# Kernel tuning notes

Hardware: AMD Instinct MI355X
Metric: run time of the kernel (lower is better)

The kernel has to match this reference:

```python
import jax, jax.numpy as jnp
import numpy as np

BN_EPS = 1e-5


def setup_inputs() -> dict:
    key = jax.random.key(0)
    ks = jax.random.split(key, 6)
    b, c_out, c_high = 8, 256, 512
    h1 = w1 = 64
    h2 = w2 = 32
    return {
        "fms_low": jax.random.normal(ks[0], (b, c_out, h1, w1), jnp.float32),
        "fms_high": jax.random.normal(ks[1], (b, c_high, h2, w2), jnp.float32),
        "w_conv": jax.random.normal(ks[2], (c_out, c_high), jnp.float32) * (1.0 / np.sqrt(c_high)),
        "bn_gamma": jnp.ones((c_out,), jnp.float32),
        "bn_beta": jnp.zeros((c_out,), jnp.float32),
        "bn_mean": jnp.zeros((c_out,), jnp.float32),
        "bn_var": jnp.ones((c_out,), jnp.float32),
        "fc1_w": jax.random.normal(ks[3], (c_out // 4, c_out), jnp.float32) * (1.0 / np.sqrt(c_out)),
        "fc1_b": jnp.zeros((c_out // 4,), jnp.float32),
        "fc2_w": jax.random.normal(ks[4], (c_out // 4, c_out), jnp.float32) * (1.0 / np.sqrt(c_out)),
        "fc2_b": jnp.zeros((c_out // 4,), jnp.float32),
        "scale": jax.random.normal(ks[5], (1,), jnp.float32),
    }


def reference(fms_low, fms_high, w_conv, bn_gamma, bn_beta, bn_mean, bn_var,
              fc1_w, fc1_b, fc2_w, fc2_b, scale):
    b, c, h1, w1 = fms_low.shape
    # conv_high: 1x1 conv (no bias) + BN (inference) + ReLU
    x = jnp.einsum('bchw,oc->bohw', fms_high, w_conv)  # [b, 256, h2, w2]
    inv = bn_gamma / jnp.sqrt(bn_var + BN_EPS)
    x = x * inv[None, :, None, None] + (bn_beta - bn_mean * inv)[None, :, None, None]
    x = jax.nn.relu(x)
    # raw row-major reshapes, matching torch .view(b, -1, C)
    feat_low = fms_low.reshape(b, -1, c)    # [b, N_low, 256]
    feat_high = x.reshape(b, -1, c)         # [b, N_high, 256]
    mid_low = feat_low @ fc1_w.T + fc1_b    # [b, N_low, 64]
    mid_high = feat_high @ fc2_w.T + fc2_b  # [b, N_high, 64]
    energy = jnp.einsum('bnd,bmd->bnm', mid_low, mid_high)  # [b, N_low, N_high]
    attn = jax.nn.softmax(energy, axis=-1)
    # bmm(feat_high^T, attn^T) -> [b, 256, N_low]
    mid = jnp.einsum('bmc,bnm->bcn', feat_high, attn).reshape(b, c, h1, w1)
    return scale[0] * mid
```

## Files before the change

kernel.cpp:

```cpp
#include <hip/hip_runtime.h>
#include <hip/hip_bf16.h>

typedef __bf16 v8bf __attribute__((ext_vector_type(8)));
typedef float  v4f  __attribute__((ext_vector_type(4)));

typedef __attribute__((address_space(3))) void       lds_vd;
typedef __attribute__((address_space(1))) const void gbl_vd;

#define MFMA16(a, b, c) __builtin_amdgcn_mfma_f32_16x16x32_bf16(a, b, c, 0, 0, 0)

__device__ __forceinline__ void split_hl(float v, __bf16* h, __bf16* l) {
    __bf16 hh = (__bf16)v;
    *h = hh;
    *l = (__bf16)(v - (float)hh);
}

__device__ __forceinline__ int swz_idx(int row, int col) {
    return row * 64 + ((((col >> 3) ^ (row & 7))) << 3) + (col & 7);
}
__device__ __forceinline__ const __bf16* frag_ptr(const __bf16* base, int row, int g) {
    return base + row * 64 + ((g ^ (row & 7)) << 3);
}


__global__ __launch_bounds__(256) void k_conv(
    const float* __restrict__ FH, const float* __restrict__ W,
    const float* __restrict__ gamma, const float* __restrict__ beta,
    const float* __restrict__ mean, const float* __restrict__ var,
    __bf16* __restrict__ Xhi, __bf16* __restrict__ Xlo, __bf16* __restrict__ VT)
{
    __shared__ __align__(16) __bf16 Ah[64 * 64];
    __shared__ __align__(16) __bf16 Al[64 * 64];
    __shared__ __align__(16) __bf16 Bh[64 * 64];
    __shared__ __align__(16) __bf16 Bl[64 * 64];
    __shared__ float invl[64], shl[64];

    const int tid = threadIdx.x, lane = tid & 63, w = tid >> 6;
    const int l15 = lane & 15, quad = lane >> 4;
    const int u0 = blockIdx.x * 16, o0 = blockIdx.y * 64, b = blockIdx.z;
    const float* FHb = FH + (size_t)b * 524288;

    if (tid < 64) {
        const int o = o0 + tid;
        const float iv = gamma[o] * rsqrtf(var[o] + 1e-5f);
        invl[tid] = iv;
        shl[tid] = beta[o] - mean[o] * iv;
    }

    const int ao = tid >> 2, aseg = tid & 3;
    float wreg[16], freg[16];
    {
        const float* wp = W + (size_t)(o0 + ao) * 512 + aseg * 16;
        #pragma unroll
        for (int q = 0; q < 4; ++q) {
            float4 f = ((const float4*)wp)[q];
            wreg[4*q] = f.x; wreg[4*q+1] = f.y; wreg[4*q+2] = f.z; wreg[4*q+3] = f.w;
        }
        const float* fp = FHb + (size_t)lane * 1024 + w * 256 + u0;
        #pragma unroll
        for (int q = 0; q < 4; ++q) {
            float4 f = ((const float4*)fp)[q];
            freg[4*q] = f.x; freg[4*q+1] = f.y; freg[4*q+2] = f.z; freg[4*q+3] = f.w;
        }
    }

    v4f acc[2][2];
    #pragma unroll
    for (int i = 0; i < 2; ++i)
        #pragma unroll
        for (int j = 0; j < 2; ++j) { v4f z = {0.f,0.f,0.f,0.f}; acc[i][j] = z; }
    const int oh = w >> 1, nh = w & 1;

    for (int ch = 0; ch < 8; ++ch) {
        if (ch) __syncthreads();
        #pragma unroll
        for (int z = 0; z < 2; ++z) {
            v8bf hv, lv;
            #pragma unroll
            for (int e = 0; e < 8; ++e) {
                __bf16 h, l; split_hl(wreg[8*z + e], &h, &l);
                hv[e] = h; lv[e] = l;
            }
            const int gi = (2*aseg + z) ^ (ao & 7);
            *(v8bf*)(Ah + ao*64 + (gi << 3)) = hv;
            *(v8bf*)(Al + ao*64 + (gi << 3)) = lv;
        }
        #pragma unroll
        for (int ul = 0; ul < 16; ++ul) {
            __bf16 h, l; split_hl(freg[ul], &h, &l);
            const int idx = (w*16 + ul)*64 + (((lane >> 3) ^ (ul & 7)) << 3) + (lane & 7);
            Bh[idx] = h; Bl[idx] = l;
        }
        __syncthreads();
        if (ch < 7) {
            const int c1 = (ch + 1) * 64;
            const float* wp = W + (size_t)(o0 + ao) * 512 + c1 + aseg * 16;
            #pragma unroll
            for (int q = 0; q < 4; ++q) {
                float4 f = ((const float4*)wp)[q];
                wreg[4*q] = f.x; wreg[4*q+1] = f.y; wreg[4*q+2] = f.z; wreg[4*q+3] = f.w;
            }
            const float* fp = FHb + (size_t)(c1 + lane) * 1024 + w * 256 + u0;
            #pragma unroll
            for (int q = 0; q < 4; ++q) {
                float4 f = ((const float4*)fp)[q];
                freg[4*q] = f.x; freg[4*q+1] = f.y; freg[4*q+2] = f.z; freg[4*q+3] = f.w;
            }
        }
        #pragma unroll
        for (int ks = 0; ks < 2; ++ks) {
            const int g = 4*ks + quad;
            v8bf a_h[2], a_l[2], b_h[2], b_l[2];
            #pragma unroll
            for (int i = 0; i < 2; ++i) {
                const int row = oh*32 + i*16 + l15;
                a_h[i] = *(const v8bf*)frag_ptr(Ah, row, g);
                a_l[i] = *(const v8bf*)frag_ptr(Al, row, g);
            }
            #pragma unroll
            for (int j = 0; j < 2; ++j) {
                const int row = nh*32 + j*16 + l15;
                b_h[j] = *(const v8bf*)frag_ptr(Bh, row, g);
                b_l[j] = *(const v8bf*)frag_ptr(Bl, row, g);
            }
            #pragma unroll
            for (int i = 0; i < 2; ++i)
                #pragma unroll
                for (int j = 0; j < 2; ++j) {
                    acc[i][j] = MFMA16(a_h[i], b_h[j], acc[i][j]);
                    acc[i][j] = MFMA16(a_h[i], b_l[j], acc[i][j]);
                    acc[i][j] = MFMA16(a_l[i], b_h[j], acc[i][j]);
                }
        }
    }
    __syncthreads();

    #pragma unroll
    for (int i = 0; i < 2; ++i)
        #pragma unroll
        for (int j = 0; j < 2; ++j)
            #pragma unroll
            for (int r = 0; r < 4; ++r) {
                const int row = oh*32 + i*16 + quad*4 + r;
                const int col = nh*32 + j*16 + l15;
                float v = acc[i][j][r] * invl[row] + shl[row];
                v = fmaxf(v, 0.f);
                __bf16 h, l; split_hl(v, &h, &l);
                const int idx = swz_idx(row, col);
                Ah[idx] = h; Al[idx] = l;
            }
    __syncthreads();
    {
        const int o = tid >> 2, pv = tid & 3;
        const size_t gbase = ((size_t)b*256 + o0 + o) * 1024 + pv*256 + u0;
        #pragma unroll
        for (int z = 0; z < 2; ++z) {
            const int gi = (2*pv + z) ^ (o & 7);
            v8bf h = *(v8bf*)(Ah + o*64 + (gi << 3));
            v8bf l = *(v8bf*)(Al + o*64 + (gi << 3));
            *(v8bf*)(Xhi + gbase + z*8) = h;
            *(v8bf*)(Xlo + gbase + z*8) = l;
        }
    }
    {
        const int ul = tid >> 4, s = tid & 15;
        __bf16 tmp[16];
        #pragma unroll
        for (int k = 0; k < 16; ++k) {
            const int m = s*16 + k;
            const int row = m >> 2;
            const int col = (m & 3)*16 + ul;
            tmp[k] = Ah[swz_idx(row, col)];
        }
        __bf16* vp = VT + ((size_t)b*256 + u0 + ul) * 1024 + 4*o0 + s*16;
        *(v8bf*)(vp)     = *(v8bf*)(tmp);
        *(v8bf*)(vp + 8) = *(v8bf*)(tmp + 8);
    }
}

__global__ __launch_bounds__(256) void k_proj32(
    const float* __restrict__ Feat, const float* __restrict__ Wfc,
    const float* __restrict__ bfc,
    __bf16* __restrict__ Ohi, __bf16* __restrict__ Olo)
{
    __shared__ __align__(16) __bf16 Bh[64 * 256];
    __shared__ __align__(16) __bf16 Bl[64 * 256];
    __shared__ __align__(16) __bf16 Eo[4][16 * 64];

    const int tid = threadIdx.x, lane = tid & 63, w = tid >> 6;
    const int l15 = lane & 15, quad = lane >> 4;
    const int r0 = blockIdx.x * 64;
    const int row = r0 + w*16 + l15;

    const float* ap = Feat + (size_t)row * 256 + quad * 8;
    float acur[8], anxt[8];
    {
        float4 f0 = ((const float4*)ap)[0];
        float4 f1 = ((const float4*)ap)[1];
        acur[0]=f0.x; acur[1]=f0.y; acur[2]=f0.z; acur[3]=f0.w;
        acur[4]=f1.x; acur[5]=f1.y; acur[6]=f1.z; acur[7]=f1.w;
    }

    {
        const int n = tid >> 2, q4 = tid & 3, n7 = n & 7;
        const float* wp = Wfc + (size_t)n * 256 + q4 * 64;
        #pragma unroll
        for (int z = 0; z < 8; ++z) {
            float4 f0 = ((const float4*)wp)[2*z];
            float4 f1 = ((const float4*)wp)[2*z + 1];
            float w8[8] = {f0.x, f0.y, f0.z, f0.w, f1.x, f1.y, f1.z, f1.w};
            v8bf hv, lv;
            #pragma unroll
            for (int e = 0; e < 8; ++e) {
                __bf16 h, l; split_hl(w8[e], &h, &l);
                hv[e] = h; lv[e] = l;
            }
            const int gsw = (q4*8 + z) ^ n7;
            *(v8bf*)(Bh + n*256 + gsw*8) = hv;
            *(v8bf*)(Bl + n*256 + gsw*8) = lv;
        }
    }
    __syncthreads();

    v4f acc[4];
    #pragma unroll
    for (int j = 0; j < 4; ++j) { v4f z = {0.f,0.f,0.f,0.f}; acc[j] = z; }

    const int l7 = l15 & 7;
    const __bf16* bh_base = Bh + l15*256;
    const __bf16* bl_base = Bl + l15*256;

    #pragma unroll
    for (int kc = 0; kc < 8; ++kc) {
        if (kc < 7) {
            float4 f0 = ((const float4*)(ap + (kc+1)*32))[0];
            float4 f1 = ((const float4*)(ap + (kc+1)*32))[1];
            anxt[0]=f0.x; anxt[1]=f0.y; anxt[2]=f0.z; anxt[3]=f0.w;
            anxt[4]=f1.x; anxt[5]=f1.y; anxt[6]=f1.z; anxt[7]=f1.w;
        }
        v8bf ah, al;
        #pragma unroll
        for (int e = 0; e < 8; ++e) {
            __bf16 h, l; split_hl(acur[e], &h, &l);
            ah[e] = h; al[e] = l;
        }
        const int goff = (((kc*4 + quad) ^ l7) << 3);
        #pragma unroll
        for (int j = 0; j < 4; ++j) {
            v8bf bh = *(const v8bf*)(bh_base + j*4096 + goff);
            v8bf bl = *(const v8bf*)(bl_base + j*4096 + goff);
            acc[j] = MFMA16(ah, bh, acc[j]);
            acc[j] = MFMA16(ah, bl, acc[j]);
            acc[j] = MFMA16(al, bh, acc[j]);
        }
        #pragma unroll
        for (int e = 0; e < 8; ++e) acur[e] = anxt[e];
    }

    __bf16* eo = &Eo[w][0];
    __bf16 lb[4][4];
    #pragma unroll
    for (int j = 0; j < 4; ++j) {
        const float bias = bfc[j*16 + l15];
        #pragma unroll
        for (int r = 0; r < 4; ++r) {
            __bf16 h, l; split_hl(acc[j][r] + bias, &h, &l);
            lb[j][r] = l;
            eo[swz_idx(quad*4 + r, j*16 + l15)] = h;
        }
    }
    const size_t orow = (size_t)row * 64;
    #pragma unroll
    for (int z = 0; z < 2; ++z) {
        const int gi = (2*quad + z) ^ l7;
        *(v8bf*)(Ohi + orow + quad*16 + z*8) = *(v8bf*)(eo + l15*64 + gi*8);
    }
    #pragma unroll
    for (int j = 0; j < 4; ++j)
        #pragma unroll
        for (int r = 0; r < 4; ++r)
            eo[swz_idx(quad*4 + r, j*16 + l15)] = lb[j][r];
    #pragma unroll
    for (int z = 0; z < 2; ++z) {
        const int gi = (2*quad + z) ^ l7;
        *(v8bf*)(Olo + orow + quad*16 + z*8) = *(v8bf*)(eo + l15*64 + gi*8);
    }
}

__global__ __launch_bounds__(256) void k_projbf(
    const __bf16* __restrict__ Fhi, const __bf16* __restrict__ Flo,
    const float* __restrict__ Wfc, const float* __restrict__ bfc,
    __bf16* __restrict__ Ohi, __bf16* __restrict__ Olo)
{
    __shared__ __align__(16) __bf16 Bh[64 * 256];
    __shared__ __align__(16) __bf16 Bl[64 * 256];
    __shared__ __align__(16) __bf16 Eo[4][16 * 64];

    const int tid = threadIdx.x, lane = tid & 63, w = tid >> 6;
    const int l15 = lane & 15, quad = lane >> 4;
    const int r0 = blockIdx.x * 64;
    const int row = r0 + w*16 + l15;

    const __bf16* fh = Fhi + (size_t)row * 256 + quad * 8;
    const __bf16* fl = Flo + (size_t)row * 256 + quad * 8;
    v8bf ah = *(const v8bf*)(fh);
    v8bf al = *(const v8bf*)(fl);

    {
        const int n = tid >> 2, q4 = tid & 3, n7 = n & 7;
        const float* wp = Wfc + (size_t)n * 256 + q4 * 64;
        #pragma unroll
        for (int z = 0; z < 8; ++z) {
            float4 f0 = ((const float4*)wp)[2*z];
            float4 f1 = ((const float4*)wp)[2*z + 1];
            float w8[8] = {f0.x, f0.y, f0.z, f0.w, f1.x, f1.y, f1.z, f1.w};
            v8bf hv, lv;
            #pragma unroll
            for (int e = 0; e < 8; ++e) {
                __bf16 h, l; split_hl(w8[e], &h, &l);
                hv[e] = h; lv[e] = l;
            }
            const int gsw = (q4*8 + z) ^ n7;
            *(v8bf*)(Bh + n*256 + gsw*8) = hv;
            *(v8bf*)(Bl + n*256 + gsw*8) = lv;
        }
    }
    __syncthreads();

    v4f acc[4];
    #pragma unroll
    for (int j = 0; j < 4; ++j) { v4f z = {0.f,0.f,0.f,0.f}; acc[j] = z; }

    const int l7 = l15 & 7;
    const __bf16* bh_base = Bh + l15*256;
    const __bf16* bl_base = Bl + l15*256;

    #pragma unroll
    for (int kc = 0; kc < 8; ++kc) {
        v8bf anh, anl;
        if (kc < 7) {
            anh = *(const v8bf*)(fh + (kc+1)*32);
            anl = *(const v8bf*)(fl + (kc+1)*32);
        }
        const int goff = (((kc*4 + quad) ^ l7) << 3);
        #pragma unroll
        for (int j = 0; j < 4; ++j) {
            v8bf bh = *(const v8bf*)(bh_base + j*4096 + goff);
            v8bf bl = *(const v8bf*)(bl_base + j*4096 + goff);
            acc[j] = MFMA16(ah, bh, acc[j]);
            acc[j] = MFMA16(ah, bl, acc[j]);
            acc[j] = MFMA16(al, bh, acc[j]);
        }
        if (kc < 7) { ah = anh; al = anl; }
    }

    __bf16* eo = &Eo[w][0];
    __bf16 lb[4][4];
    #pragma unroll
    for (int j = 0; j < 4; ++j) {
        const float bias = bfc[j*16 + l15];
        #pragma unroll
        for (int r = 0; r < 4; ++r) {
            __bf16 h, l; split_hl(acc[j][r] + bias, &h, &l);
            lb[j][r] = l;
            eo[swz_idx(quad*4 + r, j*16 + l15)] = h;
        }
    }
    const size_t orow = (size_t)row * 64;
    #pragma unroll
    for (int z = 0; z < 2; ++z) {
        const int gi = (2*quad + z) ^ l7;
        *(v8bf*)(Ohi + orow + quad*16 + z*8) = *(v8bf*)(eo + l15*64 + gi*8);
    }
    #pragma unroll
    for (int j = 0; j < 4; ++j)
        #pragma unroll
        for (int r = 0; r < 4; ++r)
            eo[swz_idx(quad*4 + r, j*16 + l15)] = lb[j][r];
    #pragma unroll
    for (int z = 0; z < 2; ++z) {
        const int gi = (2*quad + z) ^ l7;
        *(v8bf*)(Olo + orow + quad*16 + z*8) = *(v8bf*)(eo + l15*64 + gi*8);
    }
}

__global__ __launch_bounds__(512, 4) void k_attn(
    const __bf16* __restrict__ MLhi, const __bf16* __restrict__ MLlo,
    const __bf16* __restrict__ MHhi, const __bf16* __restrict__ MHlo,
    const __bf16* __restrict__ VT,
    const float* __restrict__ scale_p,
    float* __restrict__ out)
{
    __shared__ __align__(16) __bf16 Khi[2][32 * 64];
    __shared__ __align__(16) __bf16 Klo[2][32 * 64];
    __shared__ __align__(16) __bf16 Vs [2][256 * 32];
    __shared__ __align__(16) __bf16 Ps [2][4][16 * 32];
    __shared__ float lsh[2][4][16];

    const int tid = threadIdx.x, lane = tid & 63, w = tid >> 6;
    const int l15 = lane & 15, quad = lane >> 4;
    const int b = blockIdx.x & 7, qtb = blockIdx.x >> 3;
    const int q0 = qtb * 64;
    const int qt = w & 3, mb = w >> 2;

    v8bf qhi[2], qlo[2];
    {
        const __bf16* qp  = MLhi + ((size_t)(b*4096 + q0 + qt*16 + l15)) * 64;
        const __bf16* qlp = MLlo + ((size_t)(b*4096 + q0 + qt*16 + l15)) * 64;
        #pragma unroll
        for (int h = 0; h < 2; ++h) {
            qhi[h] = *(const v8bf*)(qp + h*32 + quad*8);
            qlo[h] = *(const v8bf*)(qlp + h*32 + quad*8);
        }
    }
    #pragma unroll
    for (int h = 0; h < 2; ++h) {
        asm volatile("" : "+v"(qhi[h]));
        asm volatile("" : "+v"(qlo[h]));
    }

    const char* Khg = (const char*)(MHhi + (size_t)b * 65536);
    const char* Klg = (const char*)(MHlo + (size_t)b * 65536);
    const char* Vg  = (const char*)(VT + (size_t)b * 262144);
    const int offK = (lane >> 3) * 128 + (((lane & 7) ^ ((lane >> 3) & 7)) << 4);
    const int offV = (lane >> 2) * 2048 + ((((lane & 3) ^ ((lane >> 3) & 3))) << 4);

    const char* kgsrc = (w < 4) ? Khg : Klg;
    const int ksub = (w & 3) * 1024;

    v4f oacc[4][2];
    #pragma unroll
    for (int t = 0; t < 4; ++t)
        #pragma unroll
        for (int cb = 0; cb < 2; ++cb) { v4f z = {0.f,0.f,0.f,0.f}; oacc[t][cb] = z; }
    float lrow[4] = {0.f, 0.f, 0.f, 0.f};

    {
        char* kdst = (char*)((w < 4) ? &Khi[0][0] : &Klo[0][0]);
        __builtin_amdgcn_global_load_lds((gbl_vd*)(kgsrc + ksub + offK),
                                         (lds_vd*)(kdst + ksub), 16, 0, 0);
        #pragma unroll
        for (int j = 0; j < 2; ++j) {
            const int i = w*2 + j;
            __builtin_amdgcn_global_load_lds((gbl_vd*)(Vg + i*32768 + offV),
                                             (lds_vd*)((char*)&Vs[0][0] + i*1024), 16, 0, 0);
        }
    }
    asm volatile("s_waitcnt vmcnt(2)\n\ts_barrier" ::: "memory");

    for (int ch = 0; ch < 32; ++ch) {
        const int cur = ch & 1, nxt = cur ^ 1;
        const int mn = ((ch < 31) ? (ch + 1) : 31) * 32;

        {
            char* kdst = (char*)((w < 4) ? &Khi[nxt][0] : &Klo[nxt][0]);
            __builtin_amdgcn_global_load_lds((gbl_vd*)(kgsrc + mn*128 + ksub + offK),
                                             (lds_vd*)(kdst + ksub), 16, 0, 0);
        }

        v4f sacc = {0.f, 0.f, 0.f, 0.f};
        __builtin_amdgcn_s_setprio(1);
        #pragma unroll
        for (int h = 0; h < 2; ++h) {
            const int row = mb*16 + l15, g = 4*h + quad;
            v8bf kh = *(const v8bf*)frag_ptr(&Khi[cur][0], row, g);
            v8bf kl = *(const v8bf*)frag_ptr(&Klo[cur][0], row, g);
            sacc = MFMA16(qhi[h], kh, sacc);
            sacc = MFMA16(qhi[h], kl, sacc);
            sacc = MFMA16(qlo[h], kh, sacc);
        }
        __builtin_amdgcn_s_setprio(0);

        #pragma unroll
        for (int r = 0; r < 4; ++r) {
            const float p = __expf(sacc[r]);
            lrow[r] += p;
            const int row = quad*4 + r;
            const int slot = (mb*2 + (l15 >> 3)) ^ ((row >> 1) & 3);
            Ps[cur][qt][row*32 + (slot << 3) + (l15 & 7)] = (__bf16)p;
        }

        if (ch) {
            const int pb = nxt;
            v8bf pa[4];
            #pragma unroll
            for (int t = 0; t < 4; ++t)
                pa[t] = *(const v8bf*)(&Ps[pb][t][0] + l15*32 + ((quad ^ ((l15 >> 1) & 3)) << 3));
            __builtin_amdgcn_s_setprio(1);
            #pragma unroll
            for (int cb = 0; cb < 2; ++cb) {
                const int vrow = w*32 + cb*16 + l15;
                v8bf vv = *(const v8bf*)(&Vs[pb][0] + vrow*32 + ((quad ^ ((vrow >> 1) & 3)) << 3));
                #pragma unroll
                for (int t = 0; t < 4; ++t)
                    oacc[t][cb] = MFMA16(pa[t], vv, oacc[t][cb]);
            }
            __builtin_amdgcn_s_setprio(0);
        }

        asm volatile("s_waitcnt lgkmcnt(0)" ::: "memory");
        #pragma unroll
        for (int j = 0; j < 2; ++j) {
            const int i = w*2 + j;
            __builtin_amdgcn_global_load_lds((gbl_vd*)(Vg + mn*2 + i*32768 + offV),
                                             (lds_vd*)((char*)&Vs[nxt][0] + i*1024), 16, 0, 0);
        }

        asm volatile("s_waitcnt vmcnt(2) lgkmcnt(0)\n\ts_barrier" ::: "memory");
    }

    {
        v8bf pa[4];
        #pragma unroll
        for (int t = 0; t < 4; ++t)
            pa[t] = *(const v8bf*)(&Ps[1][t][0] + l15*32 + ((quad ^ ((l15 >> 1) & 3)) << 3));
        #pragma unroll
        for (int cb = 0; cb < 2; ++cb) {
            const int vrow = w*32 + cb*16 + l15;
            v8bf vv = *(const v8bf*)(&Vs[1][0] + vrow*32 + ((quad ^ ((vrow >> 1) & 3)) << 3));
            #pragma unroll
            for (int t = 0; t < 4; ++t)
                oacc[t][cb] = MFMA16(pa[t], vv, oacc[t][cb]);
        }
    }

    #pragma unroll
    for (int r = 0; r < 4; ++r) {
        float s = lrow[r];
        #pragma unroll
        for (int d = 1; d < 16; d <<= 1) s += __shfl_xor(s, d, 64);
        lrow[r] = s;
    }
    if (l15 == 0) {
        #pragma unroll
        for (int r = 0; r < 4; ++r) lsh[mb][qt][quad*4 + r] = lrow[r];
    }
    __syncthreads();

    const float scl = scale_p[0];
    float inv[4][4];
    #pragma unroll
    for (int t = 0; t < 4; ++t)
        #pragma unroll
        for (int r = 0; r < 4; ++r)
            inv[t][r] = scl / (lsh[0][t][quad*4 + r] + lsh[1][t][quad*4 + r]);
    float* outb = out + (size_t)b * 256 * 4096;
    #pragma unroll
    for (int cb = 0; cb < 2; ++cb) {
        const int c = w*32 + cb*16 + l15;
        #pragma unroll
        for (int t = 0; t < 4; ++t) {
            float4 v;
            v.x = oacc[t][cb][0] * inv[t][0];
            v.y = oacc[t][cb][1] * inv[t][1];
            v.z = oacc[t][cb][2] * inv[t][2];
            v.w = oacc[t][cb][3] * inv[t][3];
            *(float4*)(outb + (size_t)c * 4096 + q0 + t*16 + quad*4) = v;
        }
    }
}

extern "C" void kernel_launch(void* const* d_in, const int* in_sizes, int n_in,
                              void* d_out, int out_size, void* d_ws, size_t ws_size,
                              hipStream_t stream)
{
    const float* fms_low  = (const float*)d_in[0];
    const float* fms_high = (const float*)d_in[1];
    const float* w_conv   = (const float*)d_in[2];
    const float* gamma    = (const float*)d_in[3];
    const float* beta     = (const float*)d_in[4];
    const float* mean     = (const float*)d_in[5];
    const float* var      = (const float*)d_in[6];
    const float* fc1_w    = (const float*)d_in[7];
    const float* fc1_b    = (const float*)d_in[8];
    const float* fc2_w    = (const float*)d_in[9];
    const float* fc2_b    = (const float*)d_in[10];
    const float* scale    = (const float*)d_in[11];
    float* out = (float*)d_out;

    __bf16* Xhi  = (__bf16*)d_ws;
    __bf16* Xlo  = Xhi  + (size_t)8*256*1024;
    __bf16* VT   = Xlo  + (size_t)8*256*1024;
    __bf16* MLhi = VT   + (size_t)8*256*1024;
    __bf16* MLlo = MLhi + (size_t)8*4096*64;
    __bf16* MHhi = MLlo + (size_t)8*4096*64;
    __bf16* MHlo = MHhi + (size_t)8*1024*64;

    k_conv<<<dim3(16, 4, 8), 256, 0, stream>>>(fms_high, w_conv, gamma, beta,
                                               mean, var, Xhi, Xlo, VT);
    k_projbf<<<dim3(128), 256, 0, stream>>>(Xhi, Xlo, fc2_w, fc2_b, MHhi, MHlo);
    k_proj32<<<dim3(512), 256, 0, stream>>>(fms_low, fc1_w, fc1_b, MLhi, MLlo);
    k_attn<<<dim3(512), 512, 0, stream>>>(MLhi, MLlo, MHhi, MHlo, VT, scale, out);
}
```

Baseline: 184.8 us.

## Merge conv and low-projection kernels into one launch; split score MFMA chains

Result: no change. 187.6 us (+1.5%).

```diff
diff --git a/kernel.cpp b/kernel.cpp
--- a/kernel.cpp
+++ b/kernel.cpp
@@ -23,267 +23,275 @@
 }
 
 
-__global__ __launch_bounds__(256) void k_conv(
+__global__ __launch_bounds__(256) void k_convproj(
     const float* __restrict__ FH, const float* __restrict__ W,
     const float* __restrict__ gamma, const float* __restrict__ beta,
     const float* __restrict__ mean, const float* __restrict__ var,
-    __bf16* __restrict__ Xhi, __bf16* __restrict__ Xlo, __bf16* __restrict__ VT)
+    __bf16* __restrict__ Xhi, __bf16* __restrict__ Xlo, __bf16* __restrict__ VT,
+    const float* __restrict__ Feat, const float* __restrict__ W1,
+    const float* __restrict__ b1,
+    __bf16* __restrict__ MLhi, __bf16* __restrict__ MLlo)
 {
-    __shared__ __align__(16) __bf16 Ah[64 * 64];
-    __shared__ __align__(16) __bf16 Al[64 * 64];
-    __shared__ __align__(16) __bf16 Bh[64 * 64];
-    __shared__ __align__(16) __bf16 Bl[64 * 64];
-    __shared__ float invl[64], shl[64];
+    union SMem {
+        struct {
+            __bf16 Ah[4096], Al[4096], Bh[4096], Bl[4096];
+            float invl[64], shl[64];
+        } c;
+        struct {
+            __bf16 Bh[16384], Bl[16384];
+            __bf16 Eo[4][1024];
+        } p;
+    };
+    __shared__ __align__(16) SMem sm;
 
     const int tid = threadIdx.x, lane = tid & 63, w = tid >> 6;
     const int l15 = lane & 15, quad = lane >> 4;
-    const int u0 = blockIdx.x * 16, o0 = blockIdx.y * 64, b = blockIdx.z;
-    const float* FHb = FH + (size_t)b * 524288;
-
-    if (tid < 64) {
-        const int o = o0 + tid;
-        const float iv = gamma[o] * rsqrtf(var[o] + 1e-5f);
-        invl[tid] = iv;
-        shl[tid] = beta[o] - mean[o] * iv;
-    }
-
-    const int ao = tid >> 2, aseg = tid & 3;
-    float wreg[16], freg[16];
-    {
-        const float* wp = W + (size_t)(o0 + ao) * 512 + aseg * 16;
-        #pragma unroll
-        for (int q = 0; q < 4; ++q) {
-            float4 f = ((const float4*)wp)[q];
-            wreg[4*q] = f.x; wreg[4*q+1] = f.y; wreg[4*q+2] = f.z; wreg[4*q+3] = f.w;
-        }
-        const float* fp = FHb + (size_t)lane * 1024 + w * 256 + u0;
-        #pragma unroll
-        for (int q = 0; q < 4; ++q) {
-            float4 f = ((const float4*)fp)[q];
-            freg[4*q] = f.x; freg[4*q+1] = f.y; freg[4*q+2] = f.z; freg[4*q+3] = f.w;
-        }
-    }
-
-    v4f acc[2][2];
-    #pragma unroll
-    for (int i = 0; i < 2; ++i)
-        #pragma unroll
-        for (int j = 0; j < 2; ++j) { v4f z = {0.f,0.f,0.f,0.f}; acc[i][j] = z; }
-    const int oh = w >> 1, nh = w & 1;
-
-    for (int ch = 0; ch < 8; ++ch) {
-        if (ch) __syncthreads();
-        #pragma unroll
-        for (int z = 0; z < 2; ++z) {
-            v8bf hv, lv;
-            #pragma unroll
-            for (int e = 0; e < 8; ++e) {
-                __bf16 h, l; split_hl(wreg[8*z + e], &h, &l);
-                hv[e] = h; lv[e] = l;
-            }
-            const int gi = (2*aseg + z) ^ (ao & 7);
-            *(v8bf*)(Ah + ao*64 + (gi << 3)) = hv;
-            *(v8bf*)(Al + ao*64 + (gi << 3)) = lv;
-        }
-        #pragma unroll
-        for (int ul = 0; ul < 16; ++ul) {
-            __bf16 h, l; split_hl(freg[ul], &h, &l);
-            const int idx = (w*16 + ul)*64 + (((lane >> 3) ^ (ul & 7)) << 3) + (lane & 7);
-            Bh[idx] = h; Bl[idx] = l;
-        }
-        __syncthreads();
-        if (ch < 7) {
-            const int c1 = (ch + 1) * 64;
-            const float* wp = W + (size_t)(o0 + ao) * 512 + c1 + aseg * 16;
+    const bool isconv = (blockIdx.x & 1) == 0;
+    const int sub = blockIdx.x >> 1;
+
+    if (isconv) {
+        __bf16* Ah = sm.c.Ah; __bf16* Al = sm.c.Al;
+        __bf16* Bh = sm.c.Bh; __bf16* Bl = sm.c.Bl;
+        float* invl = sm.c.invl; float* shl = sm.c.shl;
+
+        const int u0 = (sub & 15) * 16, o0 = ((sub >> 4) & 3) * 64, b = sub >> 6;
+        const float* FHb = FH + (size_t)b * 524288;
+
+        if (tid < 64) {
+            const int o = o0 + tid;
+            const float iv = gamma[o] * rsqrtf(var[o] + 1e-5f);
+            invl[tid] = iv;
+            shl[tid] = beta[o] - mean[o] * iv;
+        }
+
+        const int ao = tid >> 2, aseg = tid & 3;
+        float wreg[16], freg[16];
+        {
+            const float* wp = W + (size_t)(o0 + ao) * 512 + aseg * 16;
             #pragma unroll
             for (int q = 0; q < 4; ++q) {
                 float4 f = ((const float4*)wp)[q];
                 wreg[4*q] = f.x; wreg[4*q+1] = f.y; wreg[4*q+2] = f.z; wreg[4*q+3] = f.w;
             }
-            const float* fp = FHb + (size_t)(c1 + lane) * 1024 + w * 256 + u0;
+            const float* fp = FHb + (size_t)lane * 1024 + w * 256 + u0;
             #pragma unroll
             for (int q = 0; q < 4; ++q) {
                 float4 f = ((const float4*)fp)[q];
                 freg[4*q] = f.x; freg[4*q+1] = f.y; freg[4*q+2] = f.z; freg[4*q+3] = f.w;
             }
         }
-        #pragma unroll
-        for (int ks = 0; ks < 2; ++ks) {
-            const int g = 4*ks + quad;
-            v8bf a_h[2], a_l[2], b_h[2], b_l[2];
-            #pragma unroll
-            for (int i = 0; i < 2; ++i) {
-                const int row = oh*32 + i*16 + l15;
-                a_h[i] = *(const v8bf*)frag_ptr(Ah, row, g);
-                a_l[i] = *(const v8bf*)frag_ptr(Al, row, g);
-            }
-            #pragma unroll
-            for (int j = 0; j < 2; ++j) {
-                const int row = nh*32 + j*16 + l15;
-                b_h[j] = *(const v8bf*)frag_ptr(Bh, row, g);
-                b_l[j] = *(const v8bf*)frag_ptr(Bl, row, g);
-            }
-            #pragma unroll
-            for (int i = 0; i < 2; ++i)
+
+        v4f acc[2][2];
+        #pragma unroll
+        for (int i = 0; i < 2; ++i)
+            #pragma unroll
+            for (int j = 0; j < 2; ++j) { v4f z = {0.f,0.f,0.f,0.f}; acc[i][j] = z; }
+        const int oh = w >> 1, nh = w & 1;
+
+        for (int ch = 0; ch < 8; ++ch) {
+            if (ch) __syncthreads();
+            #pragma unroll
+            for (int z = 0; z < 2; ++z) {
+                v8bf hv, lv;
+                #pragma unroll
+                for (int e = 0; e < 8; ++e) {
+                    __bf16 h, l; split_hl(wreg[8*z + e], &h, &l);
+                    hv[e] = h; lv[e] = l;
+                }
+                const int gi = (2*aseg + z) ^ (ao & 7);
+                *(v8bf*)(Ah + ao*64 + (gi << 3)) = hv;
+                *(v8bf*)(Al + ao*64 + (gi << 3)) = lv;
+            }
+            #pragma unroll
+            for (int ul = 0; ul < 16; ++ul) {
+                __bf16 h, l; split_hl(freg[ul], &h, &l);
+                const int idx = (w*16 + ul)*64 + (((lane >> 3) ^ (ul & 7)) << 3) + (lane & 7);
+                Bh[idx] = h; Bl[idx] = l;
+            }
+            __syncthreads();
+            if (ch < 7) {
+                const int c1 = (ch + 1) * 64;
+                const float* wp = W + (size_t)(o0 + ao) * 512 + c1 + aseg * 16;
+                #pragma unroll
+                for (int q = 0; q < 4; ++q) {
+                    float4 f = ((const float4*)wp)[q];
+                    wreg[4*q] = f.x; wreg[4*q+1] = f.y; wreg[4*q+2] = f.z; wreg[4*q+3] = f.w;
+                }
+                const float* fp = FHb + (size_t)(c1 + lane) * 1024 + w * 256 + u0;
+                #pragma unroll
+                for (int q = 0; q < 4; ++q) {
+                    float4 f = ((const float4*)fp)[q];
+                    freg[4*q] = f.x; freg[4*q+1] = f.y; freg[4*q+2] = f.z; freg[4*q+3] = f.w;
+                }
+            }
+            #pragma unroll
+            for (int ks = 0; ks < 2; ++ks) {
+                const int g = 4*ks + quad;
+                v8bf a_h[2], a_l[2], b_h[2], b_l[2];
+                #pragma unroll
+                for (int i = 0; i < 2; ++i) {
+                    const int row = oh*32 + i*16 + l15;
+                    a_h[i] = *(const v8bf*)frag_ptr(Ah, row, g);
+                    a_l[i] = *(const v8bf*)frag_ptr(Al, row, g);
+                }
                 #pragma unroll
                 for (int j = 0; j < 2; ++j) {
-                    acc[i][j] = MFMA16(a_h[i], b_h[j], acc[i][j]);
-                    acc[i][j] = MFMA16(a_h[i], b_l[j], acc[i][j]);
-                    acc[i][j] = MFMA16(a_l[i], b_h[j], acc[i][j]);
+                    const int row = nh*32 + j*16 + l15;
+                    b_h[j] = *(const v8bf*)frag_ptr(Bh, row, g);
+                    b_l[j] = *(const v8bf*)frag_ptr(Bl, row, g);
                 }
-        }
-    }
-    __syncthreads();
-
-    #pragma unroll
-    for (int i = 0; i < 2; ++i)
-        #pragma unroll
-        for (int j = 0; j < 2; ++j)
+                #pragma unroll
+                for (int i = 0; i < 2; ++i)
+                    #pragma unroll
+                    for (int j = 0; j < 2; ++j) {
+                        acc[i][j] = MFMA16(a_h[i], b_h[j], acc[i][j]);
+                        acc[i][j] = MFMA16(a_h[i], b_l[j], acc[i][j]);
+                        acc[i][j] = MFMA16(a_l[i], b_h[j], acc[i][j]);
+                    }
+            }
+        }
+        __syncthreads();
+
+        #pragma unroll
+        for (int i = 0; i < 2; ++i)
+            #pragma unroll
+            for (int j = 0; j < 2; ++j)
+                #pragma unroll
+                for (int r = 0; r < 4; ++r) {
+                    const int row = oh*32 + i*16 + quad*4 + r;
+                    const int col = nh*32 + j*16 + l15;
+                    float v = acc[i][j][r] * invl[row] + shl[row];
+                    v = fmaxf(v, 0.f);
+                    __bf16 h, l; split_hl(v, &h, &l);
+                    const int idx = swz_idx(row, col);
+                    Ah[idx] = h; Al[idx] = l;
+                }
+        __syncthreads();
+        {
+            const int o = tid >> 2, pv = tid & 3;
+            const size_t gbase = ((size_t)b*256 + o0 + o) * 1024 + pv*256 + u0;
+            #pragma unroll
+            for (int z = 0; z < 2; ++z) {
+                const int gi = (2*pv + z) ^ (o & 7);
+                v8bf h = *(v8bf*)(Ah + o*64 + (gi << 3));
+                v8bf l = *(v8bf*)(Al + o*64 + (gi << 3));
+                *(v8bf*)(Xhi + gbase + z*8) = h;
+                *(v8bf*)(Xlo + gbase + z*8) = l;
+            }
+        }
+        {
+            const int ul = tid >> 4, s = tid & 15;
+            __bf16 tmp[16];
+            #pragma unroll
+            for (int k = 0; k < 16; ++k) {
+                const int m = s*16 + k;
+                const int row = m >> 2;
+                const int col = (m & 3)*16 + ul;
+                tmp[k] = Ah[swz_idx(row, col)];
+            }
+            __bf16* vp = VT + ((size_t)b*256 + u0 + ul) * 1024 + 4*o0 + s*16;
+            *(v8bf*)(vp)     = *(v8bf*)(tmp);
+            *(v8bf*)(vp + 8) = *(v8bf*)(tmp + 8);
+        }
+    } else {
+        __bf16* Bh = sm.p.Bh; __bf16* Bl = sm.p.Bl;
+
+        const int r0 = sub * 64;
+        const int row = r0 + w*16 + l15;
+
+        const float* ap = Feat + (size_t)row * 256 + quad * 8;
+        float acur[8], anxt[8];
+        {
+            float4 f0 = ((const float4*)ap)[0];
+            float4 f1 = ((const float4*)ap)[1];
+            acur[0]=f0.x; acur[1]=f0.y; acur[2]=f0.z; acur[3]=f0.w;
+            acur[4]=f1.x; acur[5]=f1.y; acur[6]=f1.z; acur[7]=f1.w;
+        }
+
+        {
+            const int n = tid >> 2, q4 = tid & 3, n7 = n & 7;
+            const float* wp = W1 + (size_t)n * 256 + q4 * 64;
+            #pragma unroll
+            for (int z = 0; z < 8; ++z) {
+                float4 f0 = ((const float4*)wp)[2*z];
+                float4 f1 = ((const float4*)wp)[2*z + 1];
+                float w8[8] = {f0.x, f0.y, f0.z, f0.w, f1.x, f1.y, f1.z, f1.w};
+                v8bf hv, lv;
+                #pragma unroll
+                for (int e = 0; e < 8; ++e) {
+                    __bf16 h, l; split_hl(w8[e], &h, &l);
+                    hv[e] = h; lv[e] = l;
+                }
+                const int gsw = (q4*8 + z) ^ n7;
+                *(v8bf*)(Bh + n*256 + gsw*8) = hv;
+                *(v8bf*)(Bl + n*256 + gsw*8) = lv;
+            }
+        }
+        __syncthreads();
+
+        v4f acc[4];
+        #pragma unroll
+        for (int j = 0; j < 4; ++j) { v4f z = {0.f,0.f,0.f,0.f}; acc[j] = z; }
+
+        const int l7 = l15 & 7;
+        const __bf16* bh_base = Bh + l15*256;
+        const __bf16* bl_base = Bl + l15*256;
+
+        #pragma unroll
+        for (int kc = 0; kc < 8; ++kc) {
+            if (kc < 7) {
+                float4 f0 = ((const float4*)(ap + (kc+1)*32))[0];
+                float4 f1 = ((const float4*)(ap + (kc+1)*32))[1];
+                anxt[0]=f0.x; anxt[1]=f0.y; anxt[2]=f0.z; anxt[3]=f0.w;
+                anxt[4]=f1.x; anxt[5]=f1.y; anxt[6]=f1.z; anxt[7]=f1.w;
+            }
+            v8bf ah, al;
+            #pragma unroll
+            for (int e = 0; e < 8; ++e) {
+                __bf16 h, l; split_hl(acur[e], &h, &l);
+                ah[e] = h; al[e] = l;
+            }
+            const int goff = (((kc*4 + quad) ^ l7) << 3);
+            #pragma unroll
+            for (int j = 0; j < 4; ++j) {
+                v8bf bh = *(const v8bf*)(bh_base + j*4096 + goff);
+                v8bf bl = *(const v8bf*)(bl_base + j*4096 + goff);
+                acc[j] = MFMA16(ah, bh, acc[j]);
+                acc[j] = MFMA16(ah, bl, acc[j]);
+                acc[j] = MFMA16(al, bh, acc[j]);
+            }
+            #pragma unroll
+            for (int e = 0; e < 8; ++e) acur[e] = anxt[e];
+        }
+
+        __bf16* eo = &sm.p.Eo[w][0];
+        __bf16 lb[4][4];
+        #pragma unroll
+        for (int j = 0; j < 4; ++j) {
+            const float bias = b1[j*16 + l15];
             #pragma unroll
             for (int r = 0; r < 4; ++r) {
-                const int row = oh*32 + i*16 + quad*4 + r;
-                const int col = nh*32 + j*16 + l15;
-                float v = acc[i][j][r] * invl[row] + shl[row];
-                v = fmaxf(v, 0.f);
-                __bf16 h, l; split_hl(v, &h, &l);
-                const int idx = swz_idx(row, col);
-                Ah[idx] = h; Al[idx] = l;
-            }
-    __syncthreads();
-    {
-        const int o = tid >> 2, pv = tid & 3;
-        const size_t gbase = ((size_t)b*256 + o0 + o) * 1024 + pv*256 + u0;
+                __bf16 h, l; split_hl(acc[j][r] + bias, &h, &l);
+                lb[j][r] = l;
+                eo[swz_idx(quad*4 + r, j*16 + l15)] = h;
+            }
+        }
+        const size_t orow = (size_t)row * 64;
         #pragma unroll
         for (int z = 0; z < 2; ++z) {
-            const int gi = (2*pv + z) ^ (o & 7);
-            v8bf h = *(v8bf*)(Ah + o*64 + (gi << 3));
-            v8bf l = *(v8bf*)(Al + o*64 + (gi << 3));
-            *(v8bf*)(Xhi + gbase + z*8) = h;
-            *(v8bf*)(Xlo + gbase + z*8) = l;
-        }
-    }
-    {
-        const int ul = tid >> 4, s = tid & 15;
-        __bf16 tmp[16];
-        #pragma unroll
-        for (int k = 0; k < 16; ++k) {
-            const int m = s*16 + k;
-            const int row = m >> 2;
-            const int col = (m & 3)*16 + ul;
-            tmp[k] = Ah[swz_idx(row, col)];
-        }
-        __bf16* vp = VT + ((size_t)b*256 + u0 + ul) * 1024 + 4*o0 + s*16;
-        *(v8bf*)(vp)     = *(v8bf*)(tmp);
-        *(v8bf*)(vp + 8) = *(v8bf*)(tmp + 8);
-    }
-}
-
-__global__ __launch_bounds__(256) void k_proj32(
-    const float* __restrict__ Feat, const float* __restrict__ Wfc,
-    const float* __restrict__ bfc,
-    __bf16* __restrict__ Ohi, __bf16* __restrict__ Olo)
-{
-    __shared__ __align__(16) __bf16 Bh[64 * 256];
-    __shared__ __align__(16) __bf16 Bl[64 * 256];
-    __shared__ __align__(16) __bf16 Eo[4][16 * 64];
-
-    const int tid = threadIdx.x, lane = tid & 63, w = tid >> 6;
-    const int l15 = lane & 15, quad = lane >> 4;
-    const int r0 = blockIdx.x * 64;
-    const int row = r0 + w*16 + l15;
-
-    const float* ap = Feat + (size_t)row * 256 + quad * 8;
-    float acur[8], anxt[8];
-    {
-        float4 f0 = ((const float4*)ap)[0];
-        float4 f1 = ((const float4*)ap)[1];
-        acur[0]=f0.x; acur[1]=f0.y; acur[2]=f0.z; acur[3]=f0.w;
-        acur[4]=f1.x; acur[5]=f1.y; acur[6]=f1.z; acur[7]=f1.w;
-    }
-
-    {
-        const int n = tid >> 2, q4 = tid & 3, n7 = n & 7;
-        const float* wp = Wfc + (size_t)n * 256 + q4 * 64;
-        #pragma unroll
-        for (int z = 0; z < 8; ++z) {
-            float4 f0 = ((const float4*)wp)[2*z];
-            float4 f1 = ((const float4*)wp)[2*z + 1];
-            float w8[8] = {f0.x, f0.y, f0.z, f0.w, f1.x, f1.y, f1.z, f1.w};
-            v8bf hv, lv;
-            #pragma unroll
-            for (int e = 0; e < 8; ++e) {
-                __bf16 h, l; split_hl(w8[e], &h, &l);
-                hv[e] = h; lv[e] = l;
-            }
-            const int gsw = (q4*8 + z) ^ n7;
-            *(v8bf*)(Bh + n*256 + gsw*8) = hv;
-            *(v8bf*)(Bl + n*256 + gsw*8) = lv;
-        }
-    }
-    __syncthreads();
-
-    v4f acc[4];
-    #pragma unroll
-    for (int j = 0; j < 4; ++j) { v4f z = {0.f,0.f,0.f,0.f}; acc[j] = z; }
-
-    const int l7 = l15 & 7;
-    const __bf16* bh_base = Bh + l15*256;
-    const __bf16* bl_base = Bl + l15*256;
-
-    #pragma unroll
-    for (int kc = 0; kc < 8; ++kc) {
-        if (kc < 7) {
-            float4 f0 = ((const float4*)(ap + (kc+1)*32))[0];
-            float4 f1 = ((const float4*)(ap + (kc+1)*32))[1];
-            anxt[0]=f0.x; anxt[1]=f0.y; anxt[2]=f0.z; anxt[3]=f0.w;
-            anxt[4]=f1.x; anxt[5]=f1.y; anxt[6]=f1.z; anxt[7]=f1.w;
-        }
-        v8bf ah, al;
-        #pragma unroll
-        for (int e = 0; e < 8; ++e) {
-            __bf16 h, l; split_hl(acur[e], &h, &l);
-            ah[e] = h; al[e] = l;
-        }
-        const int goff = (((kc*4 + quad) ^ l7) << 3);
-        #pragma unroll
-        for (int j = 0; j < 4; ++j) {
-            v8bf bh = *(const v8bf*)(bh_base + j*4096 + goff);
-            v8bf bl = *(const v8bf*)(bl_base + j*4096 + goff);
-            acc[j] = MFMA16(ah, bh, acc[j]);
-            acc[j] = MFMA16(ah, bl, acc[j]);
-            acc[j] = MFMA16(al, bh, acc[j]);
-        }
-        #pragma unroll
-        for (int e = 0; e < 8; ++e) acur[e] = anxt[e];
-    }
-
-    __bf16* eo = &Eo[w][0];
-    __bf16 lb[4][4];
-    #pragma unroll
-    for (int j = 0; j < 4; ++j) {
-        const float bias = bfc[j*16 + l15];
-        #pragma unroll
-        for (int r = 0; r < 4; ++r) {
-            __bf16 h, l; split_hl(acc[j][r] + bias, &h, &l);
-            lb[j][r] = l;
-            eo[swz_idx(quad*4 + r, j*16 + l15)] = h;
-        }
-    }
-    const size_t orow = (size_t)row * 64;
-    #pragma unroll
-    for (int z = 0; z < 2; ++z) {
-        const int gi = (2*quad + z) ^ l7;
-        *(v8bf*)(Ohi + orow + quad*16 + z*8) = *(v8bf*)(eo + l15*64 + gi*8);
-    }
-    #pragma unroll
-    for (int j = 0; j < 4; ++j)
-        #pragma unroll
-        for (int r = 0; r < 4; ++r)
-            eo[swz_idx(quad*4 + r, j*16 + l15)] = lb[j][r];
-    #pragma unroll
-    for (int z = 0; z < 2; ++z) {
-        const int gi = (2*quad + z) ^ l7;
-        *(v8bf*)(Olo + orow + quad*16 + z*8) = *(v8bf*)(eo + l15*64 + gi*8);
+            const int gi = (2*quad + z) ^ l7;
+            *(v8bf*)(MLhi + orow + quad*16 + z*8) = *(v8bf*)(eo + l15*64 + gi*8);
+        }
+        #pragma unroll
+        for (int j = 0; j < 4; ++j)
+            #pragma unroll
+            for (int r = 0; r < 4; ++r)
+                eo[swz_idx(quad*4 + r, j*16 + l15)] = lb[j][r];
+        #pragma unroll
+        for (int z = 0; z < 2; ++z) {
+            const int gi = (2*quad + z) ^ l7;
+            *(v8bf*)(MLlo + orow + quad*16 + z*8) = *(v8bf*)(eo + l15*64 + gi*8);
+        }
     }
 }
 
@@ -458,18 +466,23 @@
                                              (lds_vd*)(kdst + ksub), 16, 0, 0);
         }
 
-        v4f sacc = {0.f, 0.f, 0.f, 0.f};
+        v4f s0 = {0.f, 0.f, 0.f, 0.f}, s1 = {0.f, 0.f, 0.f, 0.f};
         __builtin_amdgcn_s_setprio(1);
-        #pragma unroll
-        for (int h = 0; h < 2; ++h) {
-            const int row = mb*16 + l15, g = 4*h + quad;
-            v8bf kh = *(const v8bf*)frag_ptr(&Khi[cur][0], row, g);
-            v8bf kl = *(const v8bf*)frag_ptr(&Klo[cur][0], row, g);
-            sacc = MFMA16(qhi[h], kh, sacc);
-            sacc = MFMA16(qhi[h], kl, sacc);
-            sacc = MFMA16(qlo[h], kh, sacc);
+        {
+            const int row = mb*16 + l15;
+            v8bf kh0 = *(const v8bf*)frag_ptr(&Khi[cur][0], row, quad);
+            v8bf kl0 = *(const v8bf*)frag_ptr(&Klo[cur][0], row, quad);
+            v8bf kh1 = *(const v8bf*)frag_ptr(&Khi[cur][0], row, 4 + quad);
+            v8bf kl1 = *(const v8bf*)frag_ptr(&Klo[cur][0], row, 4 + quad);
+            s0 = MFMA16(qhi[0], kh0, s0);
+            s1 = MFMA16(qhi[1], kh1, s1);
+            s0 = MFMA16(qhi[0], kl0, s0);
+            s1 = MFMA16(qhi[1], kl1, s1);
+            s0 = MFMA16(qlo[0], kh0, s0);
+            s1 = MFMA16(qlo[1], kh1, s1);
         }
         __builtin_amdgcn_s_setprio(0);
+        v4f sacc = s0 + s1;
 
         #pragma unroll
         for (int r = 0; r < 4; ++r) {
@@ -586,9 +599,9 @@
     __bf16* MHhi = MLlo + (size_t)8*4096*64;
     __bf16* MHlo = MHhi + (size_t)8*1024*64;
 
-    k_conv<<<dim3(16, 4, 8), 256, 0, stream>>>(fms_high, w_conv, gamma, beta,
-                                               mean, var, Xhi, Xlo, VT);
+    k_convproj<<<dim3(1024), 256, 0, stream>>>(fms_high, w_conv, gamma, beta,
+                                               mean, var, Xhi, Xlo, VT,
+                                               fms_low, fc1_w, fc1_b, MLhi, MLlo);
     k_projbf<<<dim3(128), 256, 0, stream>>>(Xhi, Xlo, fc2_w, fc2_b, MHhi, MHlo);
-    k_proj32<<<dim3(512), 256, 0, stream>>>(fms_low, fc1_w, fc1_b, MLhi, MLlo);
     k_attn<<<dim3(512), 512, 0, stream>>>(MLhi, MLlo, MHhi, MHlo, VT, scale, out);
 }
```
